# Kernel tuning notes

Hardware: AMD Instinct MI355X
Metric: run time of the kernel (lower is better)

The kernel has to match this reference:

```python
import jax, jax.numpy as jnp
import numpy as np

B, S, HID = 2, 2048, 1024
NH, HD = 16, 64
EPS = 1e-12


def setup_inputs() -> dict:
    key = jax.random.key(0)
    ks = jax.random.split(key, 6)
    w_scale = 1.0 / np.sqrt(HID)
    return {
        "hidden_states": jax.random.normal(ks[0], (B, S, HID), dtype=jnp.float32),
        "attention_mask": jnp.ones((B, S), dtype=jnp.float32),
        "Wq": jax.random.normal(ks[1], (HID, HID), dtype=jnp.float32) * w_scale,
        "bq": jnp.zeros((HID,), dtype=jnp.float32),
        "Wk": jax.random.normal(ks[2], (HID, HID), dtype=jnp.float32) * w_scale,
        "bk": jnp.zeros((HID,), dtype=jnp.float32),
        "Wv": jax.random.normal(ks[3], (HID, HID), dtype=jnp.float32) * w_scale,
        "bv": jnp.zeros((HID,), dtype=jnp.float32),
        "Wd": jax.random.normal(ks[4], (HID, HID), dtype=jnp.float32) * w_scale,
        "bd": jnp.zeros((HID,), dtype=jnp.float32),
        "ln_gamma": jnp.ones((HID,), dtype=jnp.float32),
        "ln_beta": jnp.zeros((HID,), dtype=jnp.float32),
    }


def _heads(x):  # [B,S,HID] -> [B,NH,S,HD]
    return x.reshape(B, S, NH, HD).transpose(0, 2, 1, 3)


def reference(hidden_states, attention_mask, Wq, bq, Wk, bk, Wv, bv, Wd, bd, ln_gamma, ln_beta):
    # pre-LayerNorm
    mu = jnp.mean(hidden_states, axis=-1, keepdims=True)
    var = jnp.mean(jnp.square(hidden_states - mu), axis=-1, keepdims=True)
    h = (hidden_states - mu) * jax.lax.rsqrt(var + EPS) * ln_gamma + ln_beta

    q = _heads(h @ Wq.T + bq)  # [B,NH,S,HD]
    k = _heads(h @ Wk.T + bk)
    v = _heads(h @ Wv.T + bv)

    # additive mask: -1000 * (1 - mask), broadcast over heads and query pos
    add_mask = -1000.0 * (1.0 - attention_mask)[:, None, None, :]  # [B,1,1,S]

    # scale applied symmetrically to q and k: sqrt(sqrt(HD)) each
    scale = np.sqrt(np.sqrt(HD)).astype(np.float32)
    scores = jnp.einsum("bhqd,bhkd->bhqk", q / scale, k / scale) + add_mask
    probs = jax.nn.softmax(scores, axis=-1)  # dropout p=0 -> identity
    ctx = jnp.einsum("bhqk,bhkd->bhqd", probs, v)  # [B,NH,S,HD]

    ctx = ctx.transpose(0, 2, 1, 3).reshape(B, S, HID)
    return ctx @ Wd.T + bd
```

## Files before the change

kernel.cpp:

```cpp
#include <hip/hip_runtime.h>
#include <hip/hip_bf16.h>
#include <math.h>

#define BATCH 2
#define SEQ   2048
#define HID   1024
#define NH    16
#define HD    64
#define MROWS (BATCH * SEQ)
#define VSTR  4160

typedef unsigned short u16;
typedef short bf16x8 __attribute__((ext_vector_type(8)));
typedef float f32x4  __attribute__((ext_vector_type(4)));

#define LOG2E 1.4426950408889634f
#define C2    (0.125f * LOG2E)
#define M2F   23.083120f

static __device__ __forceinline__ u16 f2bf(float f) {
    union { float f; unsigned int u; } v; v.f = f;
    unsigned int r = (v.u + 0x7FFF + ((v.u >> 16) & 1)) >> 16;
    return (u16)r;
}

static __device__ __forceinline__ unsigned int pk_bf16(float a, float b) {
    union { __hip_bfloat162 h; unsigned int u; } r;
    float2 f; f.x = a; f.y = b;
    r.h = __float22bfloat162_rn(f);
    return r.u;
}

static __device__ __forceinline__ f32x4 mfma16(bf16x8 a, bf16x8 b, f32x4 c) {
    return __builtin_amdgcn_mfma_f32_16x16x32_bf16(a, b, c, 0, 0, 0);
}

static __device__ __forceinline__ void ldsload16(const void* g, void* l) {
    __builtin_amdgcn_global_load_lds(
        (const __attribute__((address_space(1))) void*)(unsigned long long)(uintptr_t)g,
        (__attribute__((address_space(3))) void*)(unsigned int)(uintptr_t)l,
        16, 0, 0);
}

__global__ __launch_bounds__(256) void prep_kernel(const float* __restrict__ x,
                                                   const float* __restrict__ gamma,
                                                   const float* __restrict__ beta,
                                                   u16* __restrict__ h,
                                                   const float* __restrict__ w0,
                                                   const float* __restrict__ w1,
                                                   const float* __restrict__ w2,
                                                   const float* __restrict__ w3,
                                                   u16* o0, u16* o1, u16* o2, u16* o3,
                                                   const float* __restrict__ maskg,
                                                   float* __restrict__ m2g)
{
    __shared__ float red[8];
    const int t = threadIdx.x;
    if (blockIdx.x >= 8192) {
        const int idx = ((blockIdx.x - 8192) * 256 + t) * 4;
        const float4 m = *(const float4*)(maskg + idx);
        float4 o;
        o.x = fmaf(-1000.0f * (1.0f - m.x), LOG2E, -M2F);
        o.y = fmaf(-1000.0f * (1.0f - m.y), LOG2E, -M2F);
        o.z = fmaf(-1000.0f * (1.0f - m.z), LOG2E, -M2F);
        o.w = fmaf(-1000.0f * (1.0f - m.w), LOG2E, -M2F);
        *(float4*)(m2g + idx) = o;
        return;
    }
    if (blockIdx.x < 4096) {
        const int blk = blockIdx.x;
        const int which = blk >> 10;
        const int lb = blk & 1023;
        const float* src = which == 0 ? w0 : which == 1 ? w1 : which == 2 ? w2 : w3;
        u16* dst = which == 0 ? o0 : which == 1 ? o1 : which == 2 ? o2 : o3;
        const int idx = (lb * 256 + t) * 4;
        const float4 f = *(const float4*)(src + idx);
        union { u16 s[4]; uint2 v; } p;
        p.s[0] = f2bf(f.x); p.s[1] = f2bf(f.y); p.s[2] = f2bf(f.z); p.s[3] = f2bf(f.w);
        *(uint2*)(dst + idx) = p.v;
        return;
    }
    const int row = blockIdx.x - 4096;
    const float4 xv = ((const float4*)(x + (size_t)row * HID))[t];
    float s  = xv.x + xv.y + xv.z + xv.w;
    float ss = xv.x * xv.x + xv.y * xv.y + xv.z * xv.z + xv.w * xv.w;
#pragma unroll
    for (int off = 32; off > 0; off >>= 1) {
        s  += __shfl_down(s, off);
        ss += __shfl_down(ss, off);
    }
    const int wid = t >> 6;
    if ((t & 63) == 0) { red[wid] = s; red[4 + wid] = ss; }
    __syncthreads();
    s  = red[0] + red[1] + red[2] + red[3];
    ss = red[4] + red[5] + red[6] + red[7];
    const float mu   = s * (1.0f / HID);
    const float var  = ss * (1.0f / HID) - mu * mu;
    const float rstd = rsqrtf(var + 1e-12f);
    const float4 g  = ((const float4*)gamma)[t];
    const float4 bb = ((const float4*)beta)[t];
    union { u16 s[4]; uint2 v; } p;
    p.s[0] = f2bf((xv.x - mu) * rstd * g.x + bb.x);
    p.s[1] = f2bf((xv.y - mu) * rstd * g.y + bb.y);
    p.s[2] = f2bf((xv.z - mu) * rstd * g.z + bb.z);
    p.s[3] = f2bf((xv.w - mu) * rstd * g.w + bb.w);
    ((uint2*)(h + (size_t)row * HID))[t] = p.v;
}

static __device__ __forceinline__ void gemm_core(const u16* __restrict__ A,
                                                 const u16* __restrict__ B,
                                                 int K, int bm, int bn,
                                                 u16* As, u16* Bs,
                                                 int wave, int lane,
                                                 f32x4 acc[4][4])
{
    const int l15  = lane & 15;
    const int quad = lane >> 4;
    const int wm = (wave >> 1) * 64;
    const int wn = (wave & 1) * 64;

    const int c1 = wave * 64 + lane;
    const int c2 = c1 + 256;
    const u16* A1 = A + (size_t)(bm + (c1 >> 2)) * K + (c1 & 3) * 8;
    const u16* A2 = A + (size_t)(bm + (c2 >> 2)) * K + (c2 & 3) * 8;
    const u16* B1 = B + (size_t)(bn + (c1 >> 2)) * K + (c1 & 3) * 8;
    const u16* B2 = B + (size_t)(bn + (c2 >> 2)) * K + (c2 & 3) * 8;
    const int o1 = wave * 512;
    const int o2 = 2048 + wave * 512;

    ldsload16(A1, As + o1);
    ldsload16(A2, As + o2);
    ldsload16(B1, Bs + o1);
    ldsload16(B2, Bs + o2);

    const int nstep = K >> 5;
    for (int i = 0; i < nstep; i++) {
        __syncthreads();
        const int cb = (i & 1) * 4096;
        if (i + 1 < nstep) {
            const int nb = ((i + 1) & 1) * 4096;
            const int k0 = (i + 1) * 32;
            ldsload16(A1 + k0, As + nb + o1);
            ldsload16(A2 + k0, As + nb + o2);
            ldsload16(B1 + k0, Bs + nb + o1);
            ldsload16(B2 + k0, Bs + nb + o2);
        }
        bf16x8 af[4], bfr[4];
#pragma unroll
        for (int mt = 0; mt < 4; mt++)
            af[mt] = *(const bf16x8*)&As[cb + (wm + mt * 16 + l15) * 32 + quad * 8];
#pragma unroll
        for (int nt = 0; nt < 4; nt++)
            bfr[nt] = *(const bf16x8*)&Bs[cb + (wn + nt * 16 + l15) * 32 + quad * 8];
#pragma unroll
        for (int mt = 0; mt < 4; mt++)
#pragma unroll
            for (int nt = 0; nt < 4; nt++)
                acc[mt][nt] = mfma16(af[mt], bfr[nt], acc[mt][nt]);
    }
}

__global__ __launch_bounds__(256) void qkv_gemm(const u16* __restrict__ h,
                                                const u16* __restrict__ wq,
                                                const u16* __restrict__ wk,
                                                const u16* __restrict__ wv,
                                                const float* __restrict__ bq,
                                                const float* __restrict__ bk,
                                                const float* __restrict__ bv,
                                                u16* __restrict__ qo,
                                                u16* __restrict__ ko,
                                                u16* __restrict__ vo)
{
    __shared__ u16 As[8192];
    __shared__ u16 Bs[8192];
    const int blk  = blockIdx.x;
    const int wave = threadIdx.x >> 6;
    const int lane = threadIdx.x & 63;
    const int l15  = lane & 15;
    const int quad = lane >> 4;
    const int wm = (wave >> 1) * 64;
    const int wn = (wave & 1) * 64;

    f32x4 acc[4][4];
#pragma unroll
    for (int mt = 0; mt < 4; mt++)
#pragma unroll
        for (int nt = 0; nt < 4; nt++) acc[mt][nt] = (f32x4)0.0f;

    if (blk < 512) {
        const u16* W     = (blk < 256) ? wq : wk;
        const float* bia = (blk < 256) ? bq : bk;
        u16* out         = (blk < 256) ? qo : ko;
        const int local = blk & 255;
        const int bm = (local >> 3) * 128;
        const int bn = (local & 7) * 128;
        gemm_core(h, W, HID, bm, bn, As, Bs, wave, lane, acc);

        float bv4[4];
#pragma unroll
        for (int nt = 0; nt < 4; nt++) bv4[nt] = bia[bn + wn + nt * 16 + l15];
#pragma unroll
        for (int mt = 0; mt < 4; mt++)
#pragma unroll
            for (int r = 0; r < 4; r++) {
                const int m  = bm + wm + mt * 16 + quad * 4 + r;
                const int bI = m >> 11;
                const int sI = m & (SEQ - 1);
#pragma unroll
                for (int nt = 0; nt < 4; nt++) {
                    const int n  = bn + wn + nt * 16 + l15;
                    const int hh = n >> 6;
                    const int d  = n & 63;
                    out[(((size_t)(bI * NH + hh) * SEQ + sI) << 6) + d] =
                        f2bf(acc[mt][nt][r] + bv4[nt]);
                }
            }
    } else {
        const int local = blk - 512;
        const int bm = (local & 7) * 128;
        const int bn = (local >> 3) * 128;
        gemm_core(wv, h, HID, bm, bn, As, Bs, wave, lane, acc);

#pragma unroll
        for (int mt = 0; mt < 4; mt++) {
            const f32x4 bm4 = *(const f32x4*)&bv[bm + wm + mt * 16 + quad * 4];
#pragma unroll
            for (int r = 0; r < 4; r++) {
                const int row = bm + wm + mt * 16 + quad * 4 + r;
#pragma unroll
                for (int nt = 0; nt < 4; nt++) {
                    const int col = bn + wn + nt * 16 + l15;
                    vo[(size_t)row * VSTR + col] = f2bf(acc[mt][nt][r] + bm4[r]);
                }
            }
        }
    }
}

__global__ __launch_bounds__(256) void out_gemm(const u16* __restrict__ ctx,
                                                const u16* __restrict__ wd,
                                                const float* __restrict__ bd,
                                                float* __restrict__ out)
{
    __shared__ u16 As[8192];
    __shared__ u16 Bs[8192];
    const int blk  = blockIdx.x;
    const int wave = threadIdx.x >> 6;
    const int lane = threadIdx.x & 63;
    const int l15  = lane & 15;
    const int quad = lane >> 4;
    const int wm = (wave >> 1) * 64;
    const int wn = (wave & 1) * 64;
    const int bm = (blk >> 3) * 128;
    const int bn = (blk & 7) * 128;

    f32x4 acc[4][4];
#pragma unroll
    for (int mt = 0; mt < 4; mt++)
#pragma unroll
        for (int nt = 0; nt < 4; nt++) acc[mt][nt] = (f32x4)0.0f;

    gemm_core(ctx, wd, HID, bm, bn, As, Bs, wave, lane, acc);

    float bv4[4];
#pragma unroll
    for (int nt = 0; nt < 4; nt++) bv4[nt] = bd[bn + wn + nt * 16 + l15];
#pragma unroll
    for (int mt = 0; mt < 4; mt++)
#pragma unroll
        for (int r = 0; r < 4; r++) {
            const int m = bm + wm + mt * 16 + quad * 4 + r;
#pragma unroll
            for (int nt = 0; nt < 4; nt++) {
                const int n = bn + wn + nt * 16 + l15;
                out[(size_t)m * HID + n] = acc[mt][nt][r] + bv4[nt];
            }
        }
}

__global__ __launch_bounds__(256) void attn_mfma(const u16* __restrict__ qb,
                                                 const u16* __restrict__ kb,
                                                 const u16* __restrict__ vtb,
                                                 const float* __restrict__ m2g,
                                                 u16* __restrict__ ctx)
{
    __shared__ __align__(16) char smem[41984];
    u16 (*Pw)[72] = (u16(*)[72])(smem + 32768 + (threadIdx.x >> 6) * 2304);

    const int t    = threadIdx.x;
    const int wave = t >> 6;
    const int lane = t & 63;
    const int l15  = lane & 15;
    const int quad = lane >> 4;

    const int bh = blockIdx.x & 31;
    const int qt = blockIdx.x >> 5;
    const int b  = bh >> 4;
    const int hh = bh & 15;
    const int q0 = qt * 64;

    const size_t headoff = (size_t)(b * NH + hh) * SEQ * HD;
    const u16* kbase = kb + headoff;
    const u16* vbase = vtb + (size_t)(hh * HD) * VSTR + b * SEQ;
    const float* m2b = m2g + b * SEQ;

    bf16x8 Qf[2];
    {
        const int qrow = q0 + wave * 16 + l15;
#pragma unroll
        for (int ks = 0; ks < 2; ks++)
            Qf[ks] = *(const bf16x8*)(qb + headoff + (size_t)qrow * HD + ks * 32 + quad * 8);
    }

    f32x4 O[4];
#pragma unroll
    for (int mt = 0; mt < 4; mt++) O[mt] = (f32x4)0.0f;
    float lsum = 0.0f;

    const int srow = lane >> 3;
    const int lcol = (lane & 7) ^ srow;
    const int sw0 = ((quad)     ^ (l15 & 7)) * 8;
    const int sw1 = ((quad + 4) ^ (l15 & 7)) * 8;
    const int g0 = wave * 2;

    ldsload16(kbase + (size_t)(g0 * 8 + srow) * HD + lcol * 8,      smem + g0 * 1024);
    ldsload16(kbase + (size_t)(g0 * 8 + 8 + srow) * HD + lcol * 8,  smem + g0 * 1024 + 1024);
    ldsload16(vbase + (size_t)(g0 * 8 + srow) * VSTR + lcol * 8,    smem + 16384 + g0 * 1024);
    ldsload16(vbase + (size_t)(g0 * 8 + 8 + srow) * VSTR + lcol * 8,smem + 16384 + g0 * 1024 + 1024);

    for (int i = 0; i < 32; i++) {
        __syncthreads();
        const int c0 = i * 64;
        const u16* Ks  = (const u16*)(smem + (i & 1) * 8192);
        const u16* Vts = (const u16*)(smem + 16384 + (i & 1) * 8192);
        if (i + 1 < 32) {
            const int cn = c0 + 64;
            char* nbK = smem + ((i + 1) & 1) * 8192;
            char* nbV = smem + 16384 + ((i + 1) & 1) * 8192;
            ldsload16(kbase + (size_t)(cn + g0 * 8 + srow) * HD + lcol * 8,      nbK + g0 * 1024);
            ldsload16(kbase + (size_t)(cn + g0 * 8 + 8 + srow) * HD + lcol * 8,  nbK + g0 * 1024 + 1024);
            ldsload16(vbase + (size_t)(g0 * 8 + srow) * VSTR + cn + lcol * 8,    nbV + g0 * 1024);
            ldsload16(vbase + (size_t)(g0 * 8 + 8 + srow) * VSTR + cn + lcol * 8,nbV + g0 * 1024 + 1024);
        }

        f32x4 St[4];
#pragma unroll
        for (int mt = 0; mt < 4; mt++) {
            const int rb = (mt * 16 + l15) * 64;
            const bf16x8 ka0 = *(const bf16x8*)&Ks[rb + sw0];
            const bf16x8 ka1 = *(const bf16x8*)&Ks[rb + sw1];
            f32x4 a = (f32x4)0.0f;
            a = mfma16(ka0, Qf[0], a);
            a = mfma16(ka1, Qf[1], a);
            St[mt] = a;
        }

#pragma unroll
        for (int mt = 0; mt < 4; mt++) {
            const f32x4 mv = *(const f32x4*)(m2b + c0 + mt * 16 + quad * 4);
            float p0 = __builtin_amdgcn_exp2f(fmaf(St[mt][0], C2, mv[0]));
            float p1 = __builtin_amdgcn_exp2f(fmaf(St[mt][1], C2, mv[1]));
            float p2 = __builtin_amdgcn_exp2f(fmaf(St[mt][2], C2, mv[2]));
            float p3 = __builtin_amdgcn_exp2f(fmaf(St[mt][3], C2, mv[3]));
            lsum += p0 + p1 + p2 + p3;
            uint2 w;
            w.x = pk_bf16(p0, p1);
            w.y = pk_bf16(p2, p3);
            *(uint2*)&Pw[l15][mt * 16 + quad * 4] = w;
        }

        const bf16x8 Pb0 = *(const bf16x8*)&Pw[l15][quad * 8];
        const bf16x8 Pb1 = *(const bf16x8*)&Pw[l15][32 + quad * 8];

#pragma unroll
        for (int mt = 0; mt < 4; mt++) {
            const int rb = (mt * 16 + l15) * 64;
            const bf16x8 va0 = *(const bf16x8*)&Vts[rb + sw0];
            const bf16x8 va1 = *(const bf16x8*)&Vts[rb + sw1];
            O[mt] = mfma16(va0, Pb0, O[mt]);
            O[mt] = mfma16(va1, Pb1, O[mt]);
        }
    }

    lsum += __shfl_xor(lsum, 16);
    lsum += __shfl_xor(lsum, 32);
    const float linv = 1.0f / lsum;

    __syncthreads();
    float* Ot = (float*)smem + wave * (16 * 68);
#pragma unroll
    for (int mt = 0; mt < 4; mt++) {
        f32x4 v = O[mt] * linv;
        *(f32x4*)(Ot + l15 * 68 + mt * 16 + quad * 4) = v;
    }
    __syncthreads();
    {
        const int ql  = lane >> 2;
        const int seg = lane & 3;
        const float* srcp = Ot + ql * 68 + seg * 16;
        u16* dstp = ctx + (size_t)(b * SEQ + q0 + wave * 16 + ql) * HID
                        + hh * 64 + seg * 16;
#pragma unroll
        for (int j = 0; j < 2; j++) {
            union { u16 s[8]; uint4 v; } p;
#pragma unroll
            for (int i = 0; i < 8; i++) p.s[i] = f2bf(srcp[j * 8 + i]);
            *(uint4*)(dstp + j * 8) = p.v;
        }
    }
}

extern "C" void kernel_launch(void* const* d_in, const int* in_sizes, int n_in,
                              void* d_out, int out_size, void* d_ws, size_t ws_size,
                              hipStream_t stream)
{
    const float* hs    = (const float*)d_in[0];
    const float* mask  = (const float*)d_in[1];
    const float* Wq    = (const float*)d_in[2];
    const float* bq    = (const float*)d_in[3];
    const float* Wk    = (const float*)d_in[4];
    const float* bk    = (const float*)d_in[5];
    const float* Wv    = (const float*)d_in[6];
    const float* bv    = (const float*)d_in[7];
    const float* Wd    = (const float*)d_in[8];
    const float* bd    = (const float*)d_in[9];
    const float* gamma = (const float*)d_in[10];
    const float* beta  = (const float*)d_in[11];
    float* out = (float*)d_out;

    const size_t NE = (size_t)MROWS * HID;
    u16* ws   = (u16*)d_ws;
    u16* h    = ws;
    u16* qbb  = ws + NE;
    u16* kbb  = qbb + NE;
    u16* vtb  = kbb + NE;
    u16* ctxb = vtb + (size_t)HID * VSTR;
    u16* wqb  = ctxb + NE;
    u16* wkb  = wqb + HID * HID;
    u16* wvb  = wkb + HID * HID;
    u16* wdb  = wvb + HID * HID;
    float* m2 = (float*)(wdb + HID * HID);

    prep_kernel<<<8196, 256, 0, stream>>>(hs, gamma, beta, h,
                                          Wq, Wk, Wv, Wd, wqb, wkb, wvb, wdb,
                                          mask, m2);

    qkv_gemm<<<768, 256, 0, stream>>>(h, wqb, wkb, wvb, bq, bk, bv, qbb, kbb, vtb);

    attn_mfma<<<1024, 256, 0, stream>>>(qbb, kbb, vtb, m2, ctxb);

    out_gemm<<<256, 256, 0, stream>>>(ctxb, wdb, bd, out);
}
```

Before: 218.6 us.

## Triple-buffer K/V LDS pipeline with vmcnt waits, LDS mask, and setprio

Moves the attention loop from double-buffered K/V staging, with a full __syncthreads each iteration, to three buffers. Loads run two tiles ahead and each iteration waits with a partial s_waitcnt vmcnt before a raw s_barrier, so global loads overlap more of the compute. The additive mask row is copied into LDS once, so global mask reads leave the inner loop. MFMA sections are wrapped in s_setprio. LDS use grows to about 65KB, which may lower occupancy, and the hand-written vmcnt counts must match the compiler's memory-op ordering.

After: 223.7 us. 1.02x slower.

```diff
diff --git a/kernel.cpp b/kernel.cpp
--- a/kernel.cpp
+++ b/kernel.cpp
@@ -284,8 +284,9 @@
                                                  const float* __restrict__ m2g,
                                                  u16* __restrict__ ctx)
 {
-    __shared__ __align__(16) char smem[41984];
-    u16 (*Pw)[72] = (u16(*)[72])(smem + 32768 + (threadIdx.x >> 6) * 2304);
+    __shared__ __align__(16) char smem[66560];
+    u16 (*Pw)[72] = (u16(*)[72])(smem + 49152 + (threadIdx.x >> 6) * 2304);
+    float* mlds = (float*)(smem + 58368);
 
     const int t    = threadIdx.x;
     const int wave = t >> 6;
@@ -304,6 +305,13 @@
     const u16* vbase = vtb + (size_t)(hh * HD) * VSTR + b * SEQ;
     const float* m2b = m2g + b * SEQ;
 
+    {
+        const float4 a = ((const float4*)m2b)[t];
+        const float4 c = ((const float4*)m2b)[t + 256];
+        ((float4*)mlds)[t] = a;
+        ((float4*)mlds)[t + 256] = c;
+    }
+
     bf16x8 Qf[2];
     {
         const int qrow = q0 + wave * 16 + l15;
@@ -323,27 +331,44 @@
     const int sw1 = ((quad + 4) ^ (l15 & 7)) * 8;
     const int g0 = wave * 2;
 
-    ldsload16(kbase + (size_t)(g0 * 8 + srow) * HD + lcol * 8,      smem + g0 * 1024);
-    ldsload16(kbase + (size_t)(g0 * 8 + 8 + srow) * HD + lcol * 8,  smem + g0 * 1024 + 1024);
-    ldsload16(vbase + (size_t)(g0 * 8 + srow) * VSTR + lcol * 8,    smem + 16384 + g0 * 1024);
-    ldsload16(vbase + (size_t)(g0 * 8 + 8 + srow) * VSTR + lcol * 8,smem + 16384 + g0 * 1024 + 1024);
-
+    const u16* kp0 = kbase + (size_t)(g0 * 8 + srow) * HD + lcol * 8;
+    const u16* kp1 = kp0 + 8 * HD;
+    const u16* vp0 = vbase + (size_t)(g0 * 8 + srow) * VSTR + lcol * 8;
+    const u16* vp1 = vp0 + 8 * VSTR;
+
+    auto stage = [&](int buf) {
+        char* bK = smem + buf * 8192;
+        char* bV = smem + 24576 + buf * 8192;
+        ldsload16(kp0, bK + g0 * 1024);
+        ldsload16(kp1, bK + g0 * 1024 + 1024);
+        ldsload16(vp0, bV + g0 * 1024);
+        ldsload16(vp1, bV + g0 * 1024 + 1024);
+        kp0 += 64 * HD; kp1 += 64 * HD;
+        vp0 += 64;      vp1 += 64;
+    };
+
+    stage(0);
+    stage(1);
+    __syncthreads();
+
+    int cb = 0, pb = 2;
     for (int i = 0; i < 32; i++) {
-        __syncthreads();
+        if (i) {
+            if (i == 31) asm volatile("s_waitcnt vmcnt(0)" ::: "memory");
+            else         asm volatile("s_waitcnt vmcnt(4)" ::: "memory");
+            __builtin_amdgcn_s_barrier();
+        }
+        if (i + 2 < 32) {
+            stage(pb);
+            pb = (pb == 2) ? 0 : pb + 1;
+        }
         const int c0 = i * 64;
-        const u16* Ks  = (const u16*)(smem + (i & 1) * 8192);
-        const u16* Vts = (const u16*)(smem + 16384 + (i & 1) * 8192);
-        if (i + 1 < 32) {
-            const int cn = c0 + 64;
-            char* nbK = smem + ((i + 1) & 1) * 8192;
-            char* nbV = smem + 16384 + ((i + 1) & 1) * 8192;
-            ldsload16(kbase + (size_t)(cn + g0 * 8 + srow) * HD + lcol * 8,      nbK + g0 * 1024);
-            ldsload16(kbase + (size_t)(cn + g0 * 8 + 8 + srow) * HD + lcol * 8,  nbK + g0 * 1024 + 1024);
-            ldsload16(vbase + (size_t)(g0 * 8 + srow) * VSTR + cn + lcol * 8,    nbV + g0 * 1024);
-            ldsload16(vbase + (size_t)(g0 * 8 + 8 + srow) * VSTR + cn + lcol * 8,nbV + g0 * 1024 + 1024);
-        }
+        const u16* Ks  = (const u16*)(smem + cb * 8192);
+        const u16* Vts = (const u16*)(smem + 24576 + cb * 8192);
+        cb = (cb == 2) ? 0 : cb + 1;
 
         f32x4 St[4];
+        __builtin_amdgcn_s_setprio(1);
 #pragma unroll
         for (int mt = 0; mt < 4; mt++) {
             const int rb = (mt * 16 + l15) * 64;
@@ -354,10 +379,11 @@
             a = mfma16(ka1, Qf[1], a);
             St[mt] = a;
         }
+        __builtin_amdgcn_s_setprio(0);
 
 #pragma unroll
         for (int mt = 0; mt < 4; mt++) {
-            const f32x4 mv = *(const f32x4*)(m2b + c0 + mt * 16 + quad * 4);
+            const f32x4 mv = *(const f32x4*)(mlds + c0 + mt * 16 + quad * 4);
             float p0 = __builtin_amdgcn_exp2f(fmaf(St[mt][0], C2, mv[0]));
             float p1 = __builtin_amdgcn_exp2f(fmaf(St[mt][1], C2, mv[1]));
             float p2 = __builtin_amdgcn_exp2f(fmaf(St[mt][2], C2, mv[2]));
@@ -372,6 +398,7 @@
         const bf16x8 Pb0 = *(const bf16x8*)&Pw[l15][quad * 8];
         const bf16x8 Pb1 = *(const bf16x8*)&Pw[l15][32 + quad * 8];
 
+        __builtin_amdgcn_s_setprio(1);
 #pragma unroll
         for (int mt = 0; mt < 4; mt++) {
             const int rb = (mt * 16 + l15) * 64;
@@ -380,6 +407,7 @@
             O[mt] = mfma16(va0, Pb0, O[mt]);
             O[mt] = mfma16(va1, Pb1, O[mt]);
         }
+        __builtin_amdgcn_s_setprio(0);
     }
 
     lsum += __shfl_xor(lsum, 16);
```

## Double attention query tile per block and move mask and row-sum work

Applied to the files above, without the earlier changes.

The attention kernel now runs 512-thread blocks that each cover 128 query rows instead of 64. Each K/V tile loaded into LDS is therefore shared by eight waves, halving global K/V traffic per query, and each wave issues one async load per tile instead of two. The additive mask row is staged once into LDS rather than read from global memory every iteration. The softmax denominator is now accumulated with an MFMA against a ones vector instead of scalar adds and cross-lane shuffles, and s_setprio is raised around the MFMA sections. The trade-offs are more LDS per block, which may reduce occupancy, and half as many blocks in the grid.

Result: faster. 205.0 us (-6.2%).

```diff
diff --git a/kernel.cpp b/kernel.cpp
--- a/kernel.cpp
+++ b/kernel.cpp
@@ -278,14 +278,15 @@
         }
 }
 
-__global__ __launch_bounds__(256) void attn_mfma(const u16* __restrict__ qb,
-                                                 const u16* __restrict__ kb,
-                                                 const u16* __restrict__ vtb,
-                                                 const float* __restrict__ m2g,
-                                                 u16* __restrict__ ctx)
-{
-    __shared__ __align__(16) char smem[41984];
+__global__ __launch_bounds__(512, 4) void attn_mfma(const u16* __restrict__ qb,
+                                                    const u16* __restrict__ kb,
+                                                    const u16* __restrict__ vtb,
+                                                    const float* __restrict__ m2g,
+                                                    u16* __restrict__ ctx)
+{
+    __shared__ __align__(16) char smem[59392];
     u16 (*Pw)[72] = (u16(*)[72])(smem + 32768 + (threadIdx.x >> 6) * 2304);
+    float* mlds = (float*)(smem + 51200);
 
     const int t    = threadIdx.x;
     const int wave = t >> 6;
@@ -297,13 +298,15 @@
     const int qt = blockIdx.x >> 5;
     const int b  = bh >> 4;
     const int hh = bh & 15;
-    const int q0 = qt * 64;
+    const int q0 = qt * 128;
 
     const size_t headoff = (size_t)(b * NH + hh) * SEQ * HD;
     const u16* kbase = kb + headoff;
     const u16* vbase = vtb + (size_t)(hh * HD) * VSTR + b * SEQ;
     const float* m2b = m2g + b * SEQ;
 
+    ((float4*)mlds)[t] = ((const float4*)m2b)[t];
+
     bf16x8 Qf[2];
     {
         const int qrow = q0 + wave * 16 + l15;
@@ -315,18 +318,21 @@
     f32x4 O[4];
 #pragma unroll
     for (int mt = 0; mt < 4; mt++) O[mt] = (f32x4)0.0f;
-    float lsum = 0.0f;
+    f32x4 Lacc = (f32x4)0.0f;
+    bf16x8 ones;
+#pragma unroll
+    for (int j = 0; j < 8; j++) ones[j] = (short)0x3F80;
 
     const int srow = lane >> 3;
     const int lcol = (lane & 7) ^ srow;
     const int sw0 = ((quad)     ^ (l15 & 7)) * 8;
     const int sw1 = ((quad + 4) ^ (l15 & 7)) * 8;
-    const int g0 = wave * 2;
-
-    ldsload16(kbase + (size_t)(g0 * 8 + srow) * HD + lcol * 8,      smem + g0 * 1024);
-    ldsload16(kbase + (size_t)(g0 * 8 + 8 + srow) * HD + lcol * 8,  smem + g0 * 1024 + 1024);
-    ldsload16(vbase + (size_t)(g0 * 8 + srow) * VSTR + lcol * 8,    smem + 16384 + g0 * 1024);
-    ldsload16(vbase + (size_t)(g0 * 8 + 8 + srow) * VSTR + lcol * 8,smem + 16384 + g0 * 1024 + 1024);
+
+    const u16* kp = kbase + (size_t)(wave * 8 + srow) * HD + lcol * 8;
+    const u16* vp = vbase + (size_t)(wave * 8 + srow) * VSTR + lcol * 8;
+
+    ldsload16(kp, smem + wave * 1024);
+    ldsload16(vp, smem + 16384 + wave * 1024);
 
     for (int i = 0; i < 32; i++) {
         __syncthreads();
@@ -337,13 +343,12 @@
             const int cn = c0 + 64;
             char* nbK = smem + ((i + 1) & 1) * 8192;
             char* nbV = smem + 16384 + ((i + 1) & 1) * 8192;
-            ldsload16(kbase + (size_t)(cn + g0 * 8 + srow) * HD + lcol * 8,      nbK + g0 * 1024);
-            ldsload16(kbase + (size_t)(cn + g0 * 8 + 8 + srow) * HD + lcol * 8,  nbK + g0 * 1024 + 1024);
-            ldsload16(vbase + (size_t)(g0 * 8 + srow) * VSTR + cn + lcol * 8,    nbV + g0 * 1024);
-            ldsload16(vbase + (size_t)(g0 * 8 + 8 + srow) * VSTR + cn + lcol * 8,nbV + g0 * 1024 + 1024);
+            ldsload16(kp + (size_t)cn * HD, nbK + wave * 1024);
+            ldsload16(vp + cn,              nbV + wave * 1024);
         }
 
         f32x4 St[4];
+        __builtin_amdgcn_s_setprio(1);
 #pragma unroll
         for (int mt = 0; mt < 4; mt++) {
             const int rb = (mt * 16 + l15) * 64;
@@ -354,15 +359,15 @@
             a = mfma16(ka1, Qf[1], a);
             St[mt] = a;
         }
+        __builtin_amdgcn_s_setprio(0);
 
 #pragma unroll
         for (int mt = 0; mt < 4; mt++) {
-            const f32x4 mv = *(const f32x4*)(m2b + c0 + mt * 16 + quad * 4);
+            const f32x4 mv = *(const f32x4*)(mlds + c0 + mt * 16 + quad * 4);
             float p0 = __builtin_amdgcn_exp2f(fmaf(St[mt][0], C2, mv[0]));
             float p1 = __builtin_amdgcn_exp2f(fmaf(St[mt][1], C2, mv[1]));
             float p2 = __builtin_amdgcn_exp2f(fmaf(St[mt][2], C2, mv[2]));
             float p3 = __builtin_amdgcn_exp2f(fmaf(St[mt][3], C2, mv[3]));
-            lsum += p0 + p1 + p2 + p3;
             uint2 w;
             w.x = pk_bf16(p0, p1);
             w.y = pk_bf16(p2, p3);
@@ -372,6 +377,7 @@
         const bf16x8 Pb0 = *(const bf16x8*)&Pw[l15][quad * 8];
         const bf16x8 Pb1 = *(const bf16x8*)&Pw[l15][32 + quad * 8];
 
+        __builtin_amdgcn_s_setprio(1);
 #pragma unroll
         for (int mt = 0; mt < 4; mt++) {
             const int rb = (mt * 16 + l15) * 64;
@@ -380,11 +386,12 @@
             O[mt] = mfma16(va0, Pb0, O[mt]);
             O[mt] = mfma16(va1, Pb1, O[mt]);
         }
-    }
-
-    lsum += __shfl_xor(lsum, 16);
-    lsum += __shfl_xor(lsum, 32);
-    const float linv = 1.0f / lsum;
+        Lacc = mfma16(ones, Pb0, Lacc);
+        Lacc = mfma16(ones, Pb1, Lacc);
+        __builtin_amdgcn_s_setprio(0);
+    }
+
+    const float linv = 1.0f / Lacc[0];
 
     __syncthreads();
     float* Ot = (float*)smem + wave * (16 * 68);
@@ -447,7 +454,7 @@
 
     qkv_gemm<<<768, 256, 0, stream>>>(h, wqb, wkb, wvb, bq, bk, bv, qbb, kbb, vtb);
 
-    attn_mfma<<<1024, 256, 0, stream>>>(qbb, kbb, vtb, m2, ctxb);
+    attn_mfma<<<512, 512, 0, stream>>>(qbb, kbb, vtb, m2, ctxb);
 
     out_gemm<<<256, 256, 0, stream>>>(ctxb, wdb, bd, out);
 }
```
